# Performance work log

Measured on AMD Instinct MI355X. Metric: run time of the kernel, lower is better.

The kernel has to match this reference:

```python
import jax, jax.numpy as jnp
import numpy as np

B, X, H = 2048, 1024, 1024
DR = 0.5

def setup_inputs() -> dict:
    key = jax.random.key(0)
    ks = jax.random.split(key, 21)
    std = 1.0 / np.sqrt(H)
    u = lambda k, s: jax.random.uniform(k, s, jnp.float32, -std, std)
    bern = lambda k, s: (jax.random.bernoulli(k, 1.0 - DR, s) / (1.0 - DR)).astype(jnp.float32)
    return {
        "x": jax.random.normal(ks[0], (B, X), jnp.float32),
        "h0": jax.random.normal(ks[1], (B, H), jnp.float32),
        "c0": jax.random.normal(ks[2], (B, H), jnp.float32),
        "w_xi": u(ks[3], (H, X)), "w_xf": u(ks[4], (H, X)),
        "w_xc": u(ks[5], (H, X)), "w_xo": u(ks[6], (H, X)),
        "w_hi": u(ks[7], (H, H)), "w_hf": u(ks[8], (H, H)),
        "w_hc": u(ks[9], (H, H)), "w_ho": u(ks[10], (H, H)),
        "b_i": u(ks[11], (H,)), "b_f": u(ks[12], (H,)),
        "b_c": u(ks[13], (H,)), "b_o": u(ks[14], (H,)),
        "maskHI": bern(ks[15], (B, H)), "maskHF": bern(ks[16], (B, H)),
        "maskHC": bern(ks[17], (B, H)), "maskHO": bern(ks[18], (B, H)),
        "maskC": bern(ks[19], (B, H)),
    }

def reference(x, h0, c0,
              w_xi, w_xf, w_xc, w_xo,
              w_hi, w_hf, w_hc, w_ho,
              b_i, b_f, b_c, b_o,
              maskHI, maskHF, maskHC, maskHO, maskC):
    # gal dropout: per-gate masks on recurrent input h0
    hs = jnp.stack([h0 * maskHI, h0 * maskHF, h0 * maskHC, h0 * maskHO])  # [4,B,H]
    wh = jnp.stack([w_hi, w_hf, w_hc, w_ho])                              # [4,H,H]
    wx = jnp.stack([w_xi, w_xf, w_xc, w_xo])                              # [4,H,X]
    # two batched GEMMs (F.linear uses x @ W.T)
    g = jnp.einsum('bx,gkx->gbk', x, wx) + jnp.einsum('gbh,gkh->gbk', hs, wh)
    gateI = jax.nn.sigmoid(g[0] + b_i)
    gateF = jax.nn.sigmoid(g[1] + b_f)
    gateC = jnp.tanh(g[2] + b_c) * maskC   # sem dropout on candidate
    gateO = jax.nn.sigmoid(g[3] + b_o)
    c1 = gateF * c0 + gateI * gateC
    h1 = gateO * jnp.tanh(c1)
    return (h1, c1)
```

## Files before the change

### kernel.cpp

```cpp
#include <hip/hip_runtime.h>
#include <hip/hip_bf16.h>
#include <stdint.h>

#define BDIM 2048
#define HDIM 1024
#define XDIM 1024
#define BH (BDIM*HDIM)
#define WSEG 1048576

typedef __attribute__((ext_vector_type(8))) short short8;
typedef __attribute__((ext_vector_type(4))) float float4v;

__device__ __forceinline__ void gload16(const void* g, void* l) {
    __builtin_amdgcn_global_load_lds(
        (const __attribute__((address_space(1))) unsigned int*)g,
        (__attribute__((address_space(3))) unsigned int*)l, 16, 0, 0);
}

__device__ __forceinline__ unsigned pack2(float a, float b) {
    __hip_bfloat162 v = __float22bfloat162_rn(make_float2(a, b));
    return *reinterpret_cast<unsigned*>(&v);
}
__device__ __forceinline__ uint2 pack4(float4 f) {
    return make_uint2(pack2(f.x, f.y), pack2(f.z, f.w));
}
__device__ __forceinline__ float2 up2(unsigned u) {
    __hip_bfloat162 v = *reinterpret_cast<__hip_bfloat162*>(&u);
    return __bfloat1622float2(v);
}

__global__ __launch_bounds__(256) void prep_all_k(
    const float* __restrict__ w0, const float* __restrict__ w1,
    const float* __restrict__ w2, const float* __restrict__ w3,
    const float* __restrict__ w4, const float* __restrict__ w5,
    const float* __restrict__ w6, const float* __restrict__ w7,
    const float* __restrict__ x, const float* __restrict__ h0,
    const float* __restrict__ mI, const float* __restrict__ mF,
    const float* __restrict__ mC, const float* __restrict__ mO,
    uint2* __restrict__ dst) {
    const int seg = blockIdx.y;
    const int i = blockIdx.x * 256 + threadIdx.x;
    float4 f;
    if (seg < 10) {
        const float* base;
        switch (seg) {
            case 0: base = w0; break; case 1: base = w1; break;
            case 2: base = w2; break; case 3: base = w3; break;
            case 4: base = w4; break; case 5: base = w5; break;
            case 6: base = w6; break; case 7: base = w7; break;
            default: base = x + (size_t)(seg - 8) * WSEG; break;
        }
        f = ((const float4*)base)[i];
    } else {
        const int s = seg - 10;
        const int g = s >> 1, half = s & 1;
        const float* mp = (g == 0) ? mI : (g == 1) ? mF : (g == 2) ? mC : mO;
        float4 h = ((const float4*)(h0 + (size_t)half * WSEG))[i];
        float4 m = ((const float4*)(mp + (size_t)half * WSEG))[i];
        f = make_float4(h.x * m.x, h.y * m.y, h.z * m.z, h.w * m.w);
    }
    dst[(size_t)seg * (WSEG / 4) + i] = pack4(f);
}


#define BARRIER() asm volatile("s_barrier" ::: "memory")

__device__ __forceinline__ void stage_half(const __hip_bfloat16* __restrict__ gp,
                                           short* lb, int t) {
    const int r0 = t >> 3;
    const int c0 = (t & 7) ^ (r0 & 7);
    gload16(gp + (size_t)r0 * 1024 + c0 * 8, (char*)lb + t * 16);
    const int r1 = r0 + 64;
    const int c1 = (t & 7) ^ (r1 & 7);
    gload16(gp + (size_t)r1 * 1024 + c1 * 8, (char*)lb + t * 16 + 8192);
}

template<int P>
__device__ __forceinline__ void read_bf(const short8* L8, int wn_i, int lrow, int quad,
                                        short8 (&bfr)[4][2]) {
    const int bb8 = 4096 + P * 2048 + (wn_i >> 1) * 1024;
#pragma unroll
    for (int nt = 0; nt < 4; ++nt) {
        const int rb = (wn_i & 1) * 64 + nt * 16 + lrow;
#pragma unroll
        for (int ks = 0; ks < 2; ++ks)
            bfr[nt][ks] = L8[bb8 + (rb << 3) + ((ks * 4 + quad) ^ (rb & 7))];
    }
}

template<int P, int Q>
__device__ __forceinline__ void read_af(const short8* L8, int wm_i, int lrow, int quad,
                                        short8 (&af)[2][2]) {
    const int ab8 = P * 2048 + wm_i * 1024;
#pragma unroll
    for (int sub = 0; sub < 2; ++sub) {
        const int ra = Q * 32 + sub * 16 + lrow;
#pragma unroll
        for (int ks = 0; ks < 2; ++ks)
            af[sub][ks] = L8[ab8 + (ra << 3) + ((ks * 4 + quad) ^ (ra & 7))];
    }
}

template<int Q>
__device__ __forceinline__ void mfma_q(short8 (&af)[2][2], short8 (&bfr)[4][2],
                                       float4v (&acc)[8][4]) {
    __builtin_amdgcn_s_setprio(1);
#pragma unroll
    for (int sub = 0; sub < 2; ++sub)
#pragma unroll
        for (int nt = 0; nt < 4; ++nt)
#pragma unroll
            for (int ks = 0; ks < 2; ++ks)
                acc[2 * Q + sub][nt] = __builtin_amdgcn_mfma_f32_16x16x32_bf16(
                    af[sub][ks], bfr[nt][ks], acc[2 * Q + sub][nt], 0, 0, 0);
    __builtin_amdgcn_s_setprio(0);
}

__global__ __launch_bounds__(512, 2) void gemm_split(
    const __hip_bfloat16* __restrict__ ws18,
    __hip_bfloat16* __restrict__ part) {
    const int id = blockIdx.x;
    const int z = id & 7;
    const int w = id >> 3;
    const int by = w & 3;
    const int bx = w >> 2;
    const int g = z >> 1, half = z & 1;
    const __hip_bfloat16* Ap = half ? (ws18 + (size_t)(10 + 2 * g) * WSEG)
                                    : (ws18 + (size_t)8 * WSEG);
    const __hip_bfloat16* Bp = half ? (ws18 + (size_t)(4 + g) * WSEG)
                                    : (ws18 + (size_t)g * WSEG);

    __shared__ short lds[65536];

    const int t = threadIdx.x;
    const int m0 = bx * 256, n0 = by * 256;
    const int wid = t >> 6, lane = t & 63;
    const int wm_i = wid >> 2, wn_i = wid & 3;
    const int lrow = lane & 15, quad = lane >> 4;
    const short8* L8 = (const short8*)lds;

    float4v acc[8][4];
#pragma unroll
    for (int i = 0; i < 8; ++i)
#pragma unroll
        for (int j = 0; j < 4; ++j) acc[i][j] = (float4v){0.f, 0.f, 0.f, 0.f};

    auto stageA = [&](int k, int h) {
        stage_half(Ap + (size_t)(m0 + h * 128) * 1024 + (size_t)k * 64,
                   lds + (k & 1) * 16384 + h * 8192, t);
    };
    auto stageB = [&](int k, int h) {
        stage_half(Bp + (size_t)(n0 + h * 128) * 1024 + (size_t)k * 64,
                   lds + 32768 + (k & 1) * 16384 + h * 8192, t);
    };

    stageA(0, 0); stageA(0, 1); stageB(0, 0); stageB(0, 1); stageB(1, 0); stageB(1, 1);
    asm volatile("s_waitcnt vmcnt(4)" ::: "memory");
    BARRIER();

    auto iter_body = [&](int i, bool last) {
        const int T1 = 2 * i + 1;
        short8 bfr[4][2];
        short8 af[2][2];

        read_bf<0>(L8, wn_i, lrow, quad, bfr);
        read_af<0, 0>(L8, wm_i, lrow, quad, af);
        stageA(T1, 0);
        BARRIER(); __builtin_amdgcn_sched_barrier(0);
        mfma_q<0>(af, bfr, acc);
        BARRIER();

        read_af<0, 1>(L8, wm_i, lrow, quad, af);
        stageA(T1, 1);
        BARRIER(); __builtin_amdgcn_sched_barrier(0);
        mfma_q<1>(af, bfr, acc);
        BARRIER();

        read_af<0, 2>(L8, wm_i, lrow, quad, af);
        if (!last) stageB(T1 + 1, 0);
        BARRIER(); __builtin_amdgcn_sched_barrier(0);
        mfma_q<2>(af, bfr, acc);
        BARRIER();

        read_af<0, 3>(L8, wm_i, lrow, quad, af);
        if (!last) stageB(T1 + 1, 1);
        BARRIER(); __builtin_amdgcn_sched_barrier(0);
        mfma_q<3>(af, bfr, acc);
        if (last) asm volatile("s_waitcnt vmcnt(0)" ::: "memory");
        else      asm volatile("s_waitcnt vmcnt(4)" ::: "memory");
        BARRIER();

        read_bf<1>(L8, wn_i, lrow, quad, bfr);
        read_af<1, 0>(L8, wm_i, lrow, quad, af);
        if (!last) stageA(T1 + 1, 0);
        BARRIER(); __builtin_amdgcn_sched_barrier(0);
        mfma_q<0>(af, bfr, acc);
        BARRIER();

        read_af<1, 1>(L8, wm_i, lrow, quad, af);
        if (!last) stageA(T1 + 1, 1);
        BARRIER(); __builtin_amdgcn_sched_barrier(0);
        mfma_q<1>(af, bfr, acc);
        BARRIER();

        read_af<1, 2>(L8, wm_i, lrow, quad, af);
        if (!last) stageB(T1 + 2, 0);
        BARRIER(); __builtin_amdgcn_sched_barrier(0);
        mfma_q<2>(af, bfr, acc);
        BARRIER();

        read_af<1, 3>(L8, wm_i, lrow, quad, af);
        if (!last) stageB(T1 + 2, 1);
        BARRIER(); __builtin_amdgcn_sched_barrier(0);
        mfma_q<3>(af, bfr, acc);
        if (!last) {
            asm volatile("s_waitcnt vmcnt(4)" ::: "memory");
            BARRIER();
        }
    };

#pragma unroll 1
    for (int i = 0; i < 7; ++i) iter_body(i, false);
    iter_body(7, true);

    __hip_bfloat16* pz = part + (size_t)z * BH;
#pragma unroll
    for (int mt = 0; mt < 8; ++mt) {
        const int rowb = m0 + wm_i * 128 + mt * 16 + quad * 4;
#pragma unroll
        for (int nt = 0; nt < 4; ++nt) {
            const int col = n0 + wn_i * 64 + nt * 16 + lrow;
#pragma unroll
            for (int r = 0; r < 4; ++r)
                pz[(size_t)(rowb + r) * HDIM + col] = __float2bfloat16(acc[mt][nt][r]);
        }
    }
}

__global__ __launch_bounds__(256) void combine_k(
    const uint2* __restrict__ part,
    const float* __restrict__ bi, const float* __restrict__ bff,
    const float* __restrict__ bc, const float* __restrict__ bo,
    const float* __restrict__ c0, const float* __restrict__ mC,
    float4* __restrict__ out) {
    const int i = blockIdx.x * 256 + threadIdx.x;
    const int h4 = (i * 4 & (HDIM - 1)) >> 2;

    float gate[4][4];
#pragma unroll
    for (int g = 0; g < 4; ++g) {
        uint2 p0 = part[(size_t)(2 * g) * (BH / 4) + i];
        uint2 p1 = part[(size_t)(2 * g + 1) * (BH / 4) + i];
        float2 a0 = up2(p0.x), a1 = up2(p0.y);
        float2 b0 = up2(p1.x), b1 = up2(p1.y);
        gate[g][0] = a0.x + b0.x;
        gate[g][1] = a0.y + b0.y;
        gate[g][2] = a1.x + b1.x;
        gate[g][3] = a1.y + b1.y;
    }
    float4 vbi = ((const float4*)bi)[h4];
    float4 vbf = ((const float4*)bff)[h4];
    float4 vbc = ((const float4*)bc)[h4];
    float4 vbo = ((const float4*)bo)[h4];
    float4 vc0 = ((const float4*)c0)[i];
    float4 vmc = ((const float4*)mC)[i];
    const float* pbi = (const float*)&vbi;
    const float* pbf = (const float*)&vbf;
    const float* pbc = (const float*)&vbc;
    const float* pbo = (const float*)&vbo;
    const float* pc0 = (const float*)&vc0;
    const float* pmc = (const float*)&vmc;

    float h1[4], c1[4];
#pragma unroll
    for (int j = 0; j < 4; ++j) {
        float xi = gate[0][j] + pbi[j];
        float xf = gate[1][j] + pbf[j];
        float xc = gate[2][j] + pbc[j];
        float xo = gate[3][j] + pbo[j];
        float I = 1.f / (1.f + __expf(-xi));
        float F = 1.f / (1.f + __expf(-xf));
        float C = tanhf(xc) * pmc[j];
        float O = 1.f / (1.f + __expf(-xo));
        c1[j] = F * pc0[j] + I * C;
        h1[j] = O * tanhf(c1[j]);
    }
    out[i] = make_float4(h1[0], h1[1], h1[2], h1[3]);
    out[BH / 4 + i] = make_float4(c1[0], c1[1], c1[2], c1[3]);
}

extern "C" void kernel_launch(void* const* d_in, const int* in_sizes, int n_in,
                              void* d_out, int out_size, void* d_ws, size_t ws_size,
                              hipStream_t stream) {
    const float* x   = (const float*)d_in[0];
    const float* h0  = (const float*)d_in[1];
    const float* c0  = (const float*)d_in[2];
    const float* wxi = (const float*)d_in[3];
    const float* wxf = (const float*)d_in[4];
    const float* wxc = (const float*)d_in[5];
    const float* wxo = (const float*)d_in[6];
    const float* whi = (const float*)d_in[7];
    const float* whf = (const float*)d_in[8];
    const float* whc = (const float*)d_in[9];
    const float* who = (const float*)d_in[10];
    const float* bi  = (const float*)d_in[11];
    const float* bf  = (const float*)d_in[12];
    const float* bc  = (const float*)d_in[13];
    const float* bo  = (const float*)d_in[14];
    const float* mI  = (const float*)d_in[15];
    const float* mF  = (const float*)d_in[16];
    const float* mC  = (const float*)d_in[17];
    const float* mO  = (const float*)d_in[18];
    const float* mCell = (const float*)d_in[19];

    __hip_bfloat16* ws18 = (__hip_bfloat16*)d_ws;
    __hip_bfloat16* part = ws18 + (size_t)18 * WSEG;

    prep_all_k<<<dim3(WSEG / 4 / 256, 18), dim3(256), 0, stream>>>(
        wxi, wxf, wxc, wxo, whi, whf, whc, who, x, h0, mI, mF, mC, mO,
        (uint2*)ws18);

    gemm_split<<<dim3(256), dim3(512), 0, stream>>>(ws18, part);

    combine_k<<<dim3(BH / 4 / 256), dim3(256), 0, stream>>>(
        (const uint2*)part, bi, bf, bc, bo, c0, mCell, (float4*)d_out);
}
```

Measured before the change: 200.6 us.

## Share h0 loads across gate masks, widen combine vectors, add LDS waitcnts

The prep kernel now loads each h0 element once and writes all four masked copies, instead of reloading h0 for every gate segment. This cuts h0 reads fourfold and shrinks the grid from 18 to 12 rows. The combine kernel processes 8 elements per thread with 16-byte loads of the bf16 partials, halving its thread count. In the GEMM, explicit lgkmcnt waits are placed around the barriers before each MFMA group, which makes LDS-read completion explicit but may serialize some overlap.

```diff
diff --git a/kernel.cpp b/kernel.cpp
--- a/kernel.cpp
+++ b/kernel.cpp
@@ -40,7 +40,6 @@
     uint2* __restrict__ dst) {
     const int seg = blockIdx.y;
     const int i = blockIdx.x * 256 + threadIdx.x;
-    float4 f;
     if (seg < 10) {
         const float* base;
         switch (seg) {
@@ -50,20 +49,29 @@
             case 6: base = w6; break; case 7: base = w7; break;
             default: base = x + (size_t)(seg - 8) * WSEG; break;
         }
-        f = ((const float4*)base)[i];
+        float4 f = ((const float4*)base)[i];
+        dst[(size_t)seg * (WSEG / 4) + i] = pack4(f);
     } else {
-        const int s = seg - 10;
-        const int g = s >> 1, half = s & 1;
-        const float* mp = (g == 0) ? mI : (g == 1) ? mF : (g == 2) ? mC : mO;
-        float4 h = ((const float4*)(h0 + (size_t)half * WSEG))[i];
-        float4 m = ((const float4*)(mp + (size_t)half * WSEG))[i];
-        f = make_float4(h.x * m.x, h.y * m.y, h.z * m.z, h.w * m.w);
-    }
-    dst[(size_t)seg * (WSEG / 4) + i] = pack4(f);
+        const int hf = seg - 10;
+        float4 h  = ((const float4*)(h0 + (size_t)hf * WSEG))[i];
+        float4 mi = ((const float4*)(mI + (size_t)hf * WSEG))[i];
+        float4 mf = ((const float4*)(mF + (size_t)hf * WSEG))[i];
+        float4 mc = ((const float4*)(mC + (size_t)hf * WSEG))[i];
+        float4 mo = ((const float4*)(mO + (size_t)hf * WSEG))[i];
+        dst[(size_t)(10 + hf) * (WSEG / 4) + i] =
+            pack4(make_float4(h.x * mi.x, h.y * mi.y, h.z * mi.z, h.w * mi.w));
+        dst[(size_t)(12 + hf) * (WSEG / 4) + i] =
+            pack4(make_float4(h.x * mf.x, h.y * mf.y, h.z * mf.z, h.w * mf.w));
+        dst[(size_t)(14 + hf) * (WSEG / 4) + i] =
+            pack4(make_float4(h.x * mc.x, h.y * mc.y, h.z * mc.z, h.w * mc.w));
+        dst[(size_t)(16 + hf) * (WSEG / 4) + i] =
+            pack4(make_float4(h.x * mo.x, h.y * mo.y, h.z * mo.z, h.w * mo.w));
+    }
 }
 
 
 #define BARRIER() asm volatile("s_barrier" ::: "memory")
+#define LGKM0()   asm volatile("s_waitcnt lgkmcnt(0)" ::: "memory")
 
 __device__ __forceinline__ void stage_half(const __hip_bfloat16* __restrict__ gp,
                                            short* lb, int t) {
@@ -166,25 +174,26 @@
         read_bf<0>(L8, wn_i, lrow, quad, bfr);
         read_af<0, 0>(L8, wm_i, lrow, quad, af);
         stageA(T1, 0);
-        BARRIER(); __builtin_amdgcn_sched_barrier(0);
+        asm volatile("s_waitcnt lgkmcnt(8)" ::: "memory");
+        BARRIER(); LGKM0(); __builtin_amdgcn_sched_barrier(0);
         mfma_q<0>(af, bfr, acc);
         BARRIER();
 
         read_af<0, 1>(L8, wm_i, lrow, quad, af);
         stageA(T1, 1);
-        BARRIER(); __builtin_amdgcn_sched_barrier(0);
+        BARRIER(); LGKM0(); __builtin_amdgcn_sched_barrier(0);
         mfma_q<1>(af, bfr, acc);
         BARRIER();
 
         read_af<0, 2>(L8, wm_i, lrow, quad, af);
         if (!last) stageB(T1 + 1, 0);
-        BARRIER(); __builtin_amdgcn_sched_barrier(0);
+        BARRIER(); LGKM0(); __builtin_amdgcn_sched_barrier(0);
         mfma_q<2>(af, bfr, acc);
         BARRIER();
 
         read_af<0, 3>(L8, wm_i, lrow, quad, af);
         if (!last) stageB(T1 + 1, 1);
-        BARRIER(); __builtin_amdgcn_sched_barrier(0);
+        BARRIER(); LGKM0(); __builtin_amdgcn_sched_barrier(0);
         mfma_q<3>(af, bfr, acc);
         if (last) asm volatile("s_waitcnt vmcnt(0)" ::: "memory");
         else      asm volatile("s_waitcnt vmcnt(4)" ::: "memory");
@@ -193,25 +202,26 @@
         read_bf<1>(L8, wn_i, lrow, quad, bfr);
         read_af<1, 0>(L8, wm_i, lrow, quad, af);
         if (!last) stageA(T1 + 1, 0);
-        BARRIER(); __builtin_amdgcn_sched_barrier(0);
+        asm volatile("s_waitcnt lgkmcnt(8)" ::: "memory");
+        BARRIER(); LGKM0(); __builtin_amdgcn_sched_barrier(0);
         mfma_q<0>(af, bfr, acc);
         BARRIER();
 
         read_af<1, 1>(L8, wm_i, lrow, quad, af);
         if (!last) stageA(T1 + 1, 1);
-        BARRIER(); __builtin_amdgcn_sched_barrier(0);
+        BARRIER(); LGKM0(); __builtin_amdgcn_sched_barrier(0);
         mfma_q<1>(af, bfr, acc);
         BARRIER();
 
         read_af<1, 2>(L8, wm_i, lrow, quad, af);
         if (!last) stageB(T1 + 2, 0);
-        BARRIER(); __builtin_amdgcn_sched_barrier(0);
+        BARRIER(); LGKM0(); __builtin_amdgcn_sched_barrier(0);
         mfma_q<2>(af, bfr, acc);
         BARRIER();
 
         read_af<1, 3>(L8, wm_i, lrow, quad, af);
         if (!last) stageB(T1 + 2, 1);
-        BARRIER(); __builtin_amdgcn_sched_barrier(0);
+        BARRIER(); LGKM0(); __builtin_amdgcn_sched_barrier(0);
         mfma_q<3>(af, bfr, acc);
         if (!last) {
             asm volatile("s_waitcnt vmcnt(4)" ::: "memory");
@@ -238,55 +248,72 @@
 }
 
 __global__ __launch_bounds__(256) void combine_k(
-    const uint2* __restrict__ part,
+    const uint4* __restrict__ part,
     const float* __restrict__ bi, const float* __restrict__ bff,
     const float* __restrict__ bc, const float* __restrict__ bo,
     const float* __restrict__ c0, const float* __restrict__ mC,
     float4* __restrict__ out) {
     const int i = blockIdx.x * 256 + threadIdx.x;
-    const int h4 = (i * 4 & (HDIM - 1)) >> 2;
-
-    float gate[4][4];
+    const int hb = (i * 8) & (HDIM - 1);
+
+    float gate[4][8];
 #pragma unroll
     for (int g = 0; g < 4; ++g) {
-        uint2 p0 = part[(size_t)(2 * g) * (BH / 4) + i];
-        uint2 p1 = part[(size_t)(2 * g + 1) * (BH / 4) + i];
-        float2 a0 = up2(p0.x), a1 = up2(p0.y);
-        float2 b0 = up2(p1.x), b1 = up2(p1.y);
-        gate[g][0] = a0.x + b0.x;
-        gate[g][1] = a0.y + b0.y;
-        gate[g][2] = a1.x + b1.x;
-        gate[g][3] = a1.y + b1.y;
-    }
-    float4 vbi = ((const float4*)bi)[h4];
-    float4 vbf = ((const float4*)bff)[h4];
-    float4 vbc = ((const float4*)bc)[h4];
-    float4 vbo = ((const float4*)bo)[h4];
-    float4 vc0 = ((const float4*)c0)[i];
-    float4 vmc = ((const float4*)mC)[i];
-    const float* pbi = (const float*)&vbi;
-    const float* pbf = (const float*)&vbf;
-    const float* pbc = (const float*)&vbc;
-    const float* pbo = (const float*)&vbo;
-    const float* pc0 = (const float*)&vc0;
-    const float* pmc = (const float*)&vmc;
-
-    float h1[4], c1[4];
-#pragma unroll
-    for (int j = 0; j < 4; ++j) {
-        float xi = gate[0][j] + pbi[j];
-        float xf = gate[1][j] + pbf[j];
-        float xc = gate[2][j] + pbc[j];
-        float xo = gate[3][j] + pbo[j];
+        uint4 p0 = part[(size_t)(2 * g) * (BH / 8) + i];
+        uint4 p1 = part[(size_t)(2 * g + 1) * (BH / 8) + i];
+        float2 a, b;
+        a = up2(p0.x); b = up2(p1.x); gate[g][0] = a.x + b.x; gate[g][1] = a.y + b.y;
+        a = up2(p0.y); b = up2(p1.y); gate[g][2] = a.x + b.x; gate[g][3] = a.y + b.y;
+        a = up2(p0.z); b = up2(p1.z); gate[g][4] = a.x + b.x; gate[g][5] = a.y + b.y;
+        a = up2(p0.w); b = up2(p1.w); gate[g][6] = a.x + b.x; gate[g][7] = a.y + b.y;
+    }
+
+    float bb[4][8];
+    {
+        const float4* B;
+        float4 v0, v1;
+        B = (const float4*)(bi  + hb); v0 = B[0]; v1 = B[1];
+        bb[0][0]=v0.x; bb[0][1]=v0.y; bb[0][2]=v0.z; bb[0][3]=v0.w;
+        bb[0][4]=v1.x; bb[0][5]=v1.y; bb[0][6]=v1.z; bb[0][7]=v1.w;
+        B = (const float4*)(bff + hb); v0 = B[0]; v1 = B[1];
+        bb[1][0]=v0.x; bb[1][1]=v0.y; bb[1][2]=v0.z; bb[1][3]=v0.w;
+        bb[1][4]=v1.x; bb[1][5]=v1.y; bb[1][6]=v1.z; bb[1][7]=v1.w;
+        B = (const float4*)(bc  + hb); v0 = B[0]; v1 = B[1];
+        bb[2][0]=v0.x; bb[2][1]=v0.y; bb[2][2]=v0.z; bb[2][3]=v0.w;
+        bb[2][4]=v1.x; bb[2][5]=v1.y; bb[2][6]=v1.z; bb[2][7]=v1.w;
+        B = (const float4*)(bo  + hb); v0 = B[0]; v1 = B[1];
+        bb[3][0]=v0.x; bb[3][1]=v0.y; bb[3][2]=v0.z; bb[3][3]=v0.w;
+        bb[3][4]=v1.x; bb[3][5]=v1.y; bb[3][6]=v1.z; bb[3][7]=v1.w;
+    }
+
+    float c0a[8], mca[8];
+    {
+        float4 v0 = ((const float4*)c0)[2 * i], v1 = ((const float4*)c0)[2 * i + 1];
+        c0a[0]=v0.x; c0a[1]=v0.y; c0a[2]=v0.z; c0a[3]=v0.w;
+        c0a[4]=v1.x; c0a[5]=v1.y; c0a[6]=v1.z; c0a[7]=v1.w;
+        v0 = ((const float4*)mC)[2 * i]; v1 = ((const float4*)mC)[2 * i + 1];
+        mca[0]=v0.x; mca[1]=v0.y; mca[2]=v0.z; mca[3]=v0.w;
+        mca[4]=v1.x; mca[5]=v1.y; mca[6]=v1.z; mca[7]=v1.w;
+    }
+
+    float h1[8], c1[8];
+#pragma unroll
+    for (int j = 0; j < 8; ++j) {
+        float xi = gate[0][j] + bb[0][j];
+        float xf = gate[1][j] + bb[1][j];
+        float xc = gate[2][j] + bb[2][j];
+        float xo = gate[3][j] + bb[3][j];
         float I = 1.f / (1.f + __expf(-xi));
         float F = 1.f / (1.f + __expf(-xf));
-        float C = tanhf(xc) * pmc[j];
+        float C = tanhf(xc) * mca[j];
         float O = 1.f / (1.f + __expf(-xo));
-        c1[j] = F * pc0[j] + I * C;
+        c1[j] = F * c0a[j] + I * C;
         h1[j] = O * tanhf(c1[j]);
     }
-    out[i] = make_float4(h1[0], h1[1], h1[2], h1[3]);
-    out[BH / 4 + i] = make_float4(c1[0], c1[1], c1[2], c1[3]);
+    out[2 * i]              = make_float4(h1[0], h1[1], h1[2], h1[3]);
+    out[2 * i + 1]          = make_float4(h1[4], h1[5], h1[6], h1[7]);
+    out[BH / 4 + 2 * i]     = make_float4(c1[0], c1[1], c1[2], c1[3]);
+    out[BH / 4 + 2 * i + 1] = make_float4(c1[4], c1[5], c1[6], c1[7]);
 }
 
 extern "C" void kernel_launch(void* const* d_in, const int* in_sizes, int n_in,
@@ -316,12 +343,12 @@
     __hip_bfloat16* ws18 = (__hip_bfloat16*)d_ws;
     __hip_bfloat16* part = ws18 + (size_t)18 * WSEG;
 
-    prep_all_k<<<dim3(WSEG / 4 / 256, 18), dim3(256), 0, stream>>>(
+    prep_all_k<<<dim3(WSEG / 4 / 256, 12), dim3(256), 0, stream>>>(
         wxi, wxf, wxc, wxo, whi, whf, whc, who, x, h0, mI, mF, mC, mO,
         (uint2*)ws18);
 
     gemm_split<<<dim3(256), dim3(512), 0, stream>>>(ws18, part);
 
-    combine_k<<<dim3(BH / 4 / 256), dim3(256), 0, stream>>>(
-        (const uint2*)part, bi, bf, bc, bo, c0, mCell, (float4*)d_out);
-}
+    combine_k<<<dim3(BH / 8 / 256), dim3(256), 0, stream>>>(
+        (const uint4*)part, bi, bf, bc, bo, c0, mCell, (float4*)d_out);
+}
```

After: 205.8 us. +2.6%, slower.
